# Kernel tuning notes

Measured on AMD Instinct MI355X. Metric: run time of the kernel, lower is better.

The kernel has to match this reference:

```python
import jax, jax.numpy as jnp
import numpy as np

INNER_DIM = 512
SCALE = 1.0 / np.sqrt(INNER_DIM).astype(np.float32)  # module scales by 1/sqrt(inner_dim), not head_dim


def setup_inputs() -> dict:
    key = jax.random.key(0)
    ks = jax.random.split(key, 7)
    b, n, d = 4, 4096, 512
    s = 0.02
    return {
        "x": jax.random.normal(ks[0], (b, n, d), jnp.float32),
        "y": jax.random.normal(ks[1], (b, n, d), jnp.float32),
        "Wq": jax.random.normal(ks[2], (INNER_DIM, d), jnp.float32) * s,  # torch Linear weight [out, in]
        "Wk": jax.random.normal(ks[3], (INNER_DIM, d), jnp.float32) * s,
        "Wv": jax.random.normal(ks[4], (INNER_DIM, d), jnp.float32) * s,
        "Wo": jax.random.normal(ks[5], (d, INNER_DIM), jnp.float32) * s,
        "bo": jax.random.normal(ks[6], (d,), jnp.float32) * s,
    }


def reference(x, y, Wq, Wk, Wv, Wo, bo):
    # q, k from x; v from y (bias-free projections)
    q = jnp.einsum('bnd,id->bni', x, Wq)
    k = jnp.einsum('bnd,id->bni', x, Wk)
    v = jnp.einsum('bnd,id->bni', y, Wv)
    # full [b, n, n] scores, scaled by 1/sqrt(inner_dim)
    alpha = jnp.einsum('bik,bjk->bij', q, k) * SCALE
    alpha = jax.nn.softmax(alpha, axis=-1)
    ctx = jnp.einsum('bij,bjd->bid', alpha, v)
    out = jnp.einsum('bid,od->bio', ctx, Wo) + bo
    return out
```

## Files before the change

### kernel.cpp

```cpp
#include <hip/hip_runtime.h>
#include <hip/hip_bf16.h>


typedef unsigned short u16;
typedef __bf16 bf16x8 __attribute__((ext_vector_type(8)));
typedef float f32x4 __attribute__((ext_vector_type(4)));

#define SCALE_QK 0.044194173824159216f

__device__ __forceinline__ u16 f2bf(float f) {
    __hip_bfloat16 h = __float2bfloat16(f);
    return __builtin_bit_cast(u16, h);
}

__device__ __forceinline__ void load_lds16(const void* g, void* l) {
    __builtin_amdgcn_global_load_lds(
        (const __attribute__((address_space(1))) void*)g,
        (__attribute__((address_space(3))) void*)l, 16, 0, 0);
}

__global__ void cvt2_bf16_kernel(const float* __restrict__ s0, const float* __restrict__ s1,
                                 u16* __restrict__ dst, int n8, float scale0, float scale1) {
    int i = blockIdx.x * blockDim.x + threadIdx.x;
    const float4* s4;
    float scale;
    int j;
    if (i < n8) { s4 = (const float4*)s0; scale = scale0; j = i; }
    else        { s4 = (const float4*)s1; scale = scale1; j = i - n8; }
    float4 v0 = s4[2 * j], v1 = s4[2 * j + 1];
    union { u16 u[8]; uint4 v; } o;
    o.u[0] = f2bf(v0.x * scale); o.u[1] = f2bf(v0.y * scale);
    o.u[2] = f2bf(v0.z * scale); o.u[3] = f2bf(v0.w * scale);
    o.u[4] = f2bf(v1.x * scale); o.u[5] = f2bf(v1.y * scale);
    o.u[6] = f2bf(v1.z * scale); o.u[7] = f2bf(v1.w * scale);
    ((uint4*)dst)[i] = o.v;
}

__global__ void wvo_kernel(const float* __restrict__ Wo, const float* __restrict__ Wv,
                           u16* __restrict__ Wvob) {
    int ob = blockIdx.x * 4, t = threadIdx.x;
    float a[4][2] = {{0.f, 0.f}, {0.f, 0.f}, {0.f, 0.f}, {0.f, 0.f}};
    for (int i = 0; i < 512; ++i) {
        float v0 = Wv[i * 512 + t], v1 = Wv[i * 512 + t + 256];
#pragma unroll
        for (int r = 0; r < 4; ++r) {
            float w = Wo[(ob + r) * 512 + i];
            a[r][0] += w * v0;
            a[r][1] += w * v1;
        }
    }
#pragma unroll
    for (int r = 0; r < 4; ++r) {
        Wvob[(ob + r) * 512 + t] = f2bf(a[r][0]);
        Wvob[(ob + r) * 512 + t + 256] = f2bf(a[r][1]);
    }
}

template <int DOEXP>
__launch_bounds__(512, 2)
__global__ void gemm256_kernel(const u16* __restrict__ A, const u16* __restrict__ B,
                               u16* __restrict__ Cout, int N, int lda, int ldb,
                               long long sAz, long long sBz, long long sCz) {
    __shared__ u16 lds[8][8192];

    const int tid = threadIdx.x;
    const int wave = tid >> 6, lane = tid & 63;
    const int lr = lane & 15, lg = lane >> 4;
    const int wm = wave >> 2, wn = wave & 3;
    const int rsw = (lg ^ ((lr >> 1) & 3)) << 3;

    const int gx = gridDim.x, gy = gridDim.y;
    int bid = (blockIdx.z * gy + blockIdx.y) * gx + blockIdx.x;
    const int nwg = gx * gy * gridDim.z;
    int lgc = (bid & 7) * (nwg >> 3) + (bid >> 3);
    const int bx = lgc % gx;
    int rem = lgc / gx;
    const int by = rem % gy, z = rem / gy;
    const int row0 = by * 256, col0 = bx * 256;

    const u16* Ab = A + (size_t)z * sAz;
    const u16* Bb = B + (size_t)z * sBz;

    const int rb = lane >> 2;
    const int kg8 = ((lane & 3) ^ ((rb >> 1) & 3)) << 3;

    f32x4 acc[8][4];
#pragma unroll
    for (int i = 0; i < 8; ++i)
#pragma unroll
        for (int j = 0; j < 4; ++j) acc[i][j] = (f32x4){0.f, 0.f, 0.f, 0.f};

#define STAGE_HALF(s_, slot_)                                                     \
    {                                                                             \
        const int h_ = (s_)&3, ts_ = (s_) >> 2;                                   \
        const u16* G_ = (h_ & 1) ? Bb : Ab;                                       \
        const int pan_ = (h_ & 1) ? col0 : row0;                                  \
        const int ld_ = (h_ & 1) ? ldb : lda;                                     \
        const int kofs_ = ts_ * 64 + (h_ >> 1) * 32 + kg8;                        \
        _Pragma("unroll") for (int j_ = 0; j_ < 2; ++j_) {                        \
            int r_ = (j_ * 8 + wave) * 16 + rb;                                   \
            load_lds16(G_ + (size_t)(pan_ + r_) * ld_ + kofs_,                    \
                       &lds[slot_][(j_ * 8 + wave) * 512]);                       \
        }                                                                         \
    }

    #pragma unroll
    for (int s = 0; s < 6; ++s) STAGE_HALF(s, s);
    asm volatile("s_waitcnt vmcnt(4)");
    __builtin_amdgcn_s_barrier();

#pragma unroll
    for (int i = 0; i < 4; ++i) {
#pragma unroll
        for (int m = 0; m < 4; ++m) {
            const int sub = m & 1;
            const int tp = (m >> 1) & 1;
            const int aslot = tp * 4 + 2 * sub;
            const int bslot = aslot + 1;

            bf16x8 af[8];
#pragma unroll
            for (int f = 0; f < 8; ++f) {
                int row = wm * 128 + f * 16 + lr;
                af[f] = *(const bf16x8*)&lds[aslot][row * 32 + rsw];
            }
            bf16x8 bfr[4];
#pragma unroll
            for (int f = 0; f < 4; ++f) {
                int row = wn * 64 + f * 16 + lr;
                bfr[f] = *(const bf16x8*)&lds[bslot][row * 32 + rsw];
            }

            {
                const int s0 = 8 * i + 2 * m + 6;
                if (s0 < 32) STAGE_HALF(s0, (2 * m + 6) & 7);
                if (s0 + 1 < 32) STAGE_HALF(s0 + 1, (2 * m + 7) & 7);
            }

            __builtin_amdgcn_s_barrier();

            __builtin_amdgcn_s_setprio(1);
#pragma unroll
            for (int f = 0; f < 8; ++f)
#pragma unroll
                for (int n = 0; n < 4; ++n)
                    acc[f][n] = __builtin_amdgcn_mfma_f32_16x16x32_bf16(
                        af[f], bfr[n], acc[f][n], 0, 0, 0);
            __builtin_amdgcn_s_setprio(0);

            if (sub == 1) {
                if (i == 3 && m == 1) asm volatile("s_waitcnt vmcnt(0)");
                else                  asm volatile("s_waitcnt vmcnt(4)");
            }
            __builtin_amdgcn_s_barrier();
        }
    }
#undef STAGE_HALF

    u16* C = Cout + (size_t)z * sCz;
#pragma unroll
    for (int fm = 0; fm < 8; ++fm)
#pragma unroll
        for (int fn = 0; fn < 4; ++fn)
#pragma unroll
            for (int reg = 0; reg < 4; ++reg) {
                int r = row0 + wm * 128 + fm * 16 + lg * 4 + reg;
                int c = col0 + wn * 64 + fn * 16 + lr;
                float v = acc[fm][fn][reg];
                if (DOEXP) v = __expf(v);
                C[(size_t)r * N + c] = f2bf(v);
            }
}

__launch_bounds__(512, 2)
__global__ void pv8_kernel(const u16* __restrict__ P, const u16* __restrict__ vwT,
                           float* __restrict__ part, float* __restrict__ lpart) {
    __shared__ u16 lds[8][8192];

    const int tid = threadIdx.x;
    const int wave = tid >> 6, lane = tid & 63;
    const int lr = lane & 15, lg = lane >> 4;
    const int wm = wave >> 2, wn = wave & 3;
    const int rsw = (lg ^ ((lr >> 1) & 3)) << 3;

    int bid = blockIdx.x;
    int lgc = (bid & 7) * 32 + (bid >> 3);
    const int rp = lgc & 15;
    const int t5 = lgc >> 4;
    const int cx = t5 & 1, ks = (t5 >> 1) & 1, z = t5 >> 2;
    const int row0 = rp * 256;
    const int col0 = cx * 256;

    const u16* Ab = P + (size_t)z * 16777216 + (size_t)ks * 2048;
    const u16* Bb = vwT + (size_t)z * 2097152 + (size_t)ks * 2048;

    const int rb = lane >> 2;
    const int kg8 = ((lane & 3) ^ ((rb >> 1) & 3)) << 3;

    f32x4 acc[8][4];
#pragma unroll
    for (int i = 0; i < 8; ++i)
#pragma unroll
        for (int j = 0; j < 4; ++j) acc[i][j] = (f32x4){0.f, 0.f, 0.f, 0.f};
    float rsm[8] = {0.f, 0.f, 0.f, 0.f, 0.f, 0.f, 0.f, 0.f};

#define STAGE_HALF(s_, slot_)                                                     \
    {                                                                             \
        const int h_ = (s_)&3, ts_ = (s_) >> 2;                                   \
        const u16* G_ = (h_ & 1) ? Bb : Ab;                                       \
        const int pan_ = (h_ & 1) ? col0 : row0;                                  \
        const int kofs_ = ts_ * 64 + (h_ >> 1) * 32 + kg8;                        \
        _Pragma("unroll") for (int j_ = 0; j_ < 2; ++j_) {                        \
            int r_ = (j_ * 8 + wave) * 16 + rb;                                   \
            load_lds16(G_ + (size_t)(pan_ + r_) * 4096 + kofs_,                   \
                       &lds[slot_][(j_ * 8 + wave) * 512]);                       \
        }                                                                         \
    }

    #pragma unroll
    for (int s = 0; s < 6; ++s) STAGE_HALF(s, s);
    asm volatile("s_waitcnt vmcnt(4)");
    __builtin_amdgcn_s_barrier();

    for (int i = 0; i < 16; ++i) {
#pragma unroll
        for (int m = 0; m < 4; ++m) {
            const int sub = m & 1;
            const int tp = (m >> 1) & 1;
            const int aslot = tp * 4 + 2 * sub;
            const int bslot = aslot + 1;

            bf16x8 af[8];
#pragma unroll
            for (int f = 0; f < 8; ++f) {
                int row = wm * 128 + f * 16 + lr;
                af[f] = *(const bf16x8*)&lds[aslot][row * 32 + rsw];
            }
            bf16x8 bfr[4];
#pragma unroll
            for (int f = 0; f < 4; ++f) {
                int row = wn * 64 + f * 16 + lr;
                bfr[f] = *(const bf16x8*)&lds[bslot][row * 32 + rsw];
            }

            {
                const int s0 = 8 * i + 2 * m + 6;
                if (s0 < 128) STAGE_HALF(s0, (2 * m + 6) & 7);
                if (s0 + 1 < 128) STAGE_HALF(s0 + 1, (2 * m + 7) & 7);
            }

            __builtin_amdgcn_s_barrier();

            __builtin_amdgcn_s_setprio(1);
#pragma unroll
            for (int f = 0; f < 8; ++f)
#pragma unroll
                for (int n = 0; n < 4; ++n)
                    acc[f][n] = __builtin_amdgcn_mfma_f32_16x16x32_bf16(
                        af[f], bfr[n], acc[f][n], 0, 0, 0);
            __builtin_amdgcn_s_setprio(0);

            if (wn == 0) {
#pragma unroll
                for (int f = 0; f < 8; ++f) {
                    union { bf16x8 v; unsigned u[4]; } cv;
                    cv.v = af[f];
#pragma unroll
                    for (int w = 0; w < 4; ++w)
                        rsm[f] += __uint_as_float(cv.u[w] << 16) +
                                  __uint_as_float(cv.u[w] & 0xffff0000u);
                }
            }

            if (sub == 1) {
                if (i == 15 && m == 1) asm volatile("s_waitcnt vmcnt(0)");
                else                   asm volatile("s_waitcnt vmcnt(4)");
            }
            __builtin_amdgcn_s_barrier();
        }
    }
#undef STAGE_HALF

    if (wn == 0) {
#pragma unroll
        for (int j = 0; j < 8; ++j) {
            rsm[j] += __shfl_xor(rsm[j], 16, 64);
            rsm[j] += __shfl_xor(rsm[j], 32, 64);
        }
        if (cx == 0 && lg == 0) {
            float* lp = lpart + (size_t)ks * 16384 + z * 4096 + row0 + wm * 128;
#pragma unroll
            for (int j = 0; j < 8; ++j) lp[j * 16 + lr] = rsm[j];
        }
    }

    float* O = part + (size_t)ks * 8388608 + ((size_t)z * 4096 + row0) * 512;
#pragma unroll
    for (int fm = 0; fm < 8; ++fm)
#pragma unroll
        for (int fn = 0; fn < 4; ++fn) {
            int c = col0 + wn * 64 + fn * 16 + lr;
#pragma unroll
            for (int reg = 0; reg < 4; ++reg) {
                int r = wm * 128 + fm * 16 + lg * 4 + reg;
                O[(size_t)r * 512 + c] = acc[fm][fn][reg];
            }
        }
}

template <int EPI>
__launch_bounds__(256)
__global__ void gemm_bt_kernel(const u16* __restrict__ A, const u16* __restrict__ B,
                               void* __restrict__ Cout, int N, int K, int lda, int ldb,
                               long long sAz, long long sBz, long long sCz) {
    __shared__ u16 As[2][128 * 32];
    __shared__ u16 Bs[2][128 * 32];

    const int tid = threadIdx.x;
    const int wave = tid >> 6, lane = tid & 63;
    const int lr = lane & 15, lg = lane >> 4;
    const int wr = wave >> 1, wc = wave & 1;

    const int gx = gridDim.x, gy = gridDim.y;
    int bid = (blockIdx.z * gy + blockIdx.y) * gx + blockIdx.x;
    const int nwg = gx * gy * gridDim.z;
    int lgc = (bid & 7) * (nwg >> 3) + (bid >> 3);
    const int bx = lgc % gx;
    int rem = lgc / gx;
    const int by = rem % gy, z = rem / gy;
    const int row0 = by * 128, col0 = bx * 128;

    const u16* Ab = A + (size_t)z * sAz;
    const u16* Bb = B + (size_t)z * sBz;

    f32x4 acc[4][4];
#pragma unroll
    for (int i = 0; i < 4; ++i)
#pragma unroll
        for (int j = 0; j < 4; ++j) acc[i][j] = (f32x4){0.f, 0.f, 0.f, 0.f};

    const int KT = K >> 5;

#define STAGE(bufi, kt2)                                                          \
    {                                                                             \
        _Pragma("unroll") for (int i = 0; i < 2; ++i) {                           \
            int chunk = i * 256 + tid;                                            \
            int r = chunk >> 2, c4 = chunk & 3;                                   \
            load_lds16(Ab + (size_t)(row0 + r) * lda + (kt2) * 32 + c4 * 8,       \
                       &As[bufi][(i * 256 + wave * 64) * 8]);                     \
            load_lds16(Bb + (size_t)(col0 + r) * ldb + (kt2) * 32 + c4 * 8,       \
                       &Bs[bufi][(i * 256 + wave * 64) * 8]);                     \
        }                                                                         \
    }

    STAGE(0, 0);
    int buf = 0;
    for (int kt = 0; kt < KT; ++kt) {
        __syncthreads();
        if (kt + 1 < KT) STAGE(buf ^ 1, kt + 1);

        bf16x8 af[4], bfr[4];
#pragma unroll
        for (int mf = 0; mf < 4; ++mf)
            af[mf] = *(const bf16x8*)&As[buf][(wr * 64 + mf * 16 + lr) * 32 + lg * 8];
#pragma unroll
        for (int nf = 0; nf < 4; ++nf)
            bfr[nf] = *(const bf16x8*)&Bs[buf][(wc * 64 + nf * 16 + lr) * 32 + lg * 8];
#pragma unroll
        for (int mf = 0; mf < 4; ++mf)
#pragma unroll
            for (int nf = 0; nf < 4; ++nf)
                acc[mf][nf] = __builtin_amdgcn_mfma_f32_16x16x32_bf16(
                    af[mf], bfr[nf], acc[mf][nf], 0, 0, 0);
        buf ^= 1;
    }
#undef STAGE

    const int rbase = row0 + wr * 64;
    const int cbase = col0 + wc * 64;

    if (EPI == 0) {
        u16* C = (u16*)Cout + (size_t)z * sCz;
#pragma unroll
        for (int mf = 0; mf < 4; ++mf)
#pragma unroll
            for (int nf = 0; nf < 4; ++nf)
#pragma unroll
                for (int reg = 0; reg < 4; ++reg) {
                    int r = rbase + mf * 16 + lg * 4 + reg;
                    int c = cbase + nf * 16 + lr;
                    C[(size_t)r * N + c] = f2bf(acc[mf][nf][reg]);
                }
    } else {
        u16* C = (u16*)Cout;
#pragma unroll
        for (int mf = 0; mf < 4; ++mf)
#pragma unroll
            for (int nf = 0; nf < 4; ++nf) {
                int rg = rbase + mf * 16 + lg * 4;
                int bsel = rg >> 12, rl = rg & 4095;
                int c = cbase + nf * 16 + lr;
                union { u16 u[4]; uint2 v; } o;
#pragma unroll
                for (int reg = 0; reg < 4; ++reg) o.u[reg] = f2bf(acc[mf][nf][reg]);
                *(uint2*)(C + ((size_t)bsel << 21) + ((size_t)c << 12) + rl) = o.v;
            }
    }
}

__global__ void reduce_kernel(const float* __restrict__ part,
                              const float* __restrict__ lpart,
                              const float* __restrict__ bo,
                              float* __restrict__ out) {
    int i = blockIdx.x * blockDim.x + threadIdx.x;
    int r = i >> 7, c4 = i & 127;
    float inv = 1.0f / (lpart[r] + lpart[16384 + r]);
    float4 a = ((const float4*)part)[i];
    float4 b = ((const float4*)part)[i + 2097152];
    float4 bi = ((const float4*)bo)[c4];
    float4 o;
    o.x = (a.x + b.x) * inv + bi.x;
    o.y = (a.y + b.y) * inv + bi.y;
    o.z = (a.z + b.z) * inv + bi.z;
    o.w = (a.w + b.w) * inv + bi.w;
    ((float4*)out)[i] = o;
}

extern "C" void kernel_launch(void* const* d_in, const int* in_sizes, int n_in,
                              void* d_out, int out_size, void* d_ws, size_t ws_size,
                              hipStream_t stream) {
    const float* x  = (const float*)d_in[0];
    const float* y  = (const float*)d_in[1];
    const float* Wq = (const float*)d_in[2];
    const float* Wk = (const float*)d_in[3];
    const float* Wv = (const float*)d_in[4];
    const float* Wo = (const float*)d_in[5];
    const float* bo = (const float*)d_in[6];
    float* out = (float*)d_out;

    char* ws = (char*)d_ws;
    u16*   xb   = (u16*)(ws + 0);
    u16*   qk   = (u16*)(ws + 33554432);
    float* part = (float*)(ws + 0);
    u16*   vwT  = (u16*)(ws + 67108864);
    u16*   Wqkb = (u16*)(ws + 83886080);
    u16*   Wvob = (u16*)(ws + 84934656);
    float* lpart= (float*)(ws + 86507520);
    u16*   P    = (u16*)(ws + 86638592);

    cvt2_bf16_kernel<<<8192, 256, 0, stream>>>(x, y, xb, 1048576, 1.0f, 1.0f);
    cvt2_bf16_kernel<<<256, 256, 0, stream>>>(Wq, Wk, Wqkb, 32768, SCALE_QK, 1.0f);
    wvo_kernel<<<128, 256, 0, stream>>>(Wo, Wv, Wvob);

    gemm256_kernel<0><<<dim3(4, 64, 1), 512, 0, stream>>>(xb, Wqkb, qk,
                                                          1024, 512, 512, 0, 0, 0);
    gemm_bt_kernel<1><<<dim3(4, 128, 1), 256, 0, stream>>>(xb + 8388608, Wvob, vwT,
                                                           512, 512, 512, 512, 0, 0, 0);

    gemm256_kernel<1><<<dim3(16, 16, 4), 512, 0, stream>>>(qk, qk + 512, P,
                                                           4096, 1024, 1024,
                                                           4194304, 4194304, 16777216);

    pv8_kernel<<<256, 512, 0, stream>>>(P, vwT, part, lpart);

    reduce_kernel<<<8192, 256, 0, stream>>>(part, lpart, bo, out);
}
```

Before: 317.9 us.

## Fuse prep kernels and loop batches in QK gemm with cross-batch prefetch

Merges the two conversion kernels and the Wv·Wo precompute into one prep launch, removing two launches. The QK^T exp gemm now covers all 4 batches in one persistent 256-block grid. Each block loops over the batches and prefetches the next batch's first K stages during the current batch's tail, which hides pipeline fill and drain. This cuts grid parallelism from 1024 to 256 blocks, so there is one wave of blocks per CU with less latency hiding from oversubscription.

Result: slower. 376.4 us (+18.4%).

```diff
diff --git a/kernel.cpp b/kernel.cpp
--- a/kernel.cpp
+++ b/kernel.cpp
@@ -19,44 +19,52 @@
         (__attribute__((address_space(3))) void*)l, 16, 0, 0);
 }
 
-__global__ void cvt2_bf16_kernel(const float* __restrict__ s0, const float* __restrict__ s1,
-                                 u16* __restrict__ dst, int n8, float scale0, float scale1) {
-    int i = blockIdx.x * blockDim.x + threadIdx.x;
-    const float4* s4;
-    float scale;
-    int j;
-    if (i < n8) { s4 = (const float4*)s0; scale = scale0; j = i; }
-    else        { s4 = (const float4*)s1; scale = scale1; j = i - n8; }
-    float4 v0 = s4[2 * j], v1 = s4[2 * j + 1];
-    union { u16 u[8]; uint4 v; } o;
-    o.u[0] = f2bf(v0.x * scale); o.u[1] = f2bf(v0.y * scale);
-    o.u[2] = f2bf(v0.z * scale); o.u[3] = f2bf(v0.w * scale);
-    o.u[4] = f2bf(v1.x * scale); o.u[5] = f2bf(v1.y * scale);
-    o.u[6] = f2bf(v1.z * scale); o.u[7] = f2bf(v1.w * scale);
-    ((uint4*)dst)[i] = o.v;
-}
-
-__global__ void wvo_kernel(const float* __restrict__ Wo, const float* __restrict__ Wv,
-                           u16* __restrict__ Wvob) {
-    int ob = blockIdx.x * 4, t = threadIdx.x;
-    float a[4][2] = {{0.f, 0.f}, {0.f, 0.f}, {0.f, 0.f}, {0.f, 0.f}};
-    for (int i = 0; i < 512; ++i) {
-        float v0 = Wv[i * 512 + t], v1 = Wv[i * 512 + t + 256];
+__global__ void prep_kernel(const float* __restrict__ x, const float* __restrict__ y,
+                            const float* __restrict__ Wq, const float* __restrict__ Wk,
+                            const float* __restrict__ Wo, const float* __restrict__ Wv,
+                            u16* __restrict__ xb, u16* __restrict__ Wqkb,
+                            u16* __restrict__ Wvob) {
+    const int b = blockIdx.x, tid = threadIdx.x;
+    if (b < 8448) {
+        const float *s0, *s1;
+        u16* dst;
+        int n8, i;
+        float sc0, sc1;
+        if (b < 8192) { s0 = x;  s1 = y;  dst = xb;   n8 = 1048576; sc0 = 1.f;      sc1 = 1.f; i = b * 256 + tid; }
+        else          { s0 = Wq; s1 = Wk; dst = Wqkb; n8 = 32768;   sc0 = SCALE_QK; sc1 = 1.f; i = (b - 8192) * 256 + tid; }
+        const float4* s4;
+        float scale;
+        int j;
+        if (i < n8) { s4 = (const float4*)s0; scale = sc0; j = i; }
+        else        { s4 = (const float4*)s1; scale = sc1; j = i - n8; }
+        float4 v0 = s4[2 * j], v1 = s4[2 * j + 1];
+        union { u16 u[8]; uint4 v; } o;
+        o.u[0] = f2bf(v0.x * scale); o.u[1] = f2bf(v0.y * scale);
+        o.u[2] = f2bf(v0.z * scale); o.u[3] = f2bf(v0.w * scale);
+        o.u[4] = f2bf(v1.x * scale); o.u[5] = f2bf(v1.y * scale);
+        o.u[6] = f2bf(v1.z * scale); o.u[7] = f2bf(v1.w * scale);
+        ((uint4*)dst)[i] = o.v;
+    } else {
+        int ob = (b - 8448) * 4, t = tid;
+        float a[4][2] = {{0.f, 0.f}, {0.f, 0.f}, {0.f, 0.f}, {0.f, 0.f}};
+        for (int i = 0; i < 512; ++i) {
+            float v0 = Wv[i * 512 + t], v1 = Wv[i * 512 + t + 256];
+#pragma unroll
+            for (int r = 0; r < 4; ++r) {
+                float w = Wo[(ob + r) * 512 + i];
+                a[r][0] += w * v0;
+                a[r][1] += w * v1;
+            }
+        }
 #pragma unroll
         for (int r = 0; r < 4; ++r) {
-            float w = Wo[(ob + r) * 512 + i];
-            a[r][0] += w * v0;
-            a[r][1] += w * v1;
-        }
-    }
-#pragma unroll
-    for (int r = 0; r < 4; ++r) {
-        Wvob[(ob + r) * 512 + t] = f2bf(a[r][0]);
-        Wvob[(ob + r) * 512 + t + 256] = f2bf(a[r][1]);
-    }
-}
-
-template <int DOEXP>
+            Wvob[(ob + r) * 512 + t] = f2bf(a[r][0]);
+            Wvob[(ob + r) * 512 + t + 256] = f2bf(a[r][1]);
+        }
+    }
+}
+
+template <int DOEXP, int TPB>
 __launch_bounds__(512, 2)
 __global__ void gemm256_kernel(const u16* __restrict__ A, const u16* __restrict__ B,
                                u16* __restrict__ Cout, int N, int lda, int ldb,
@@ -70,30 +78,19 @@
     const int rsw = (lg ^ ((lr >> 1) & 3)) << 3;
 
     const int gx = gridDim.x, gy = gridDim.y;
-    int bid = (blockIdx.z * gy + blockIdx.y) * gx + blockIdx.x;
-    const int nwg = gx * gy * gridDim.z;
+    int bid = blockIdx.y * gx + blockIdx.x;
+    const int nwg = gx * gy;
     int lgc = (bid & 7) * (nwg >> 3) + (bid >> 3);
-    const int bx = lgc % gx;
-    int rem = lgc / gx;
-    const int by = rem % gy, z = rem / gy;
+    const int bx = lgc % gx, by = lgc / gx;
     const int row0 = by * 256, col0 = bx * 256;
-
-    const u16* Ab = A + (size_t)z * sAz;
-    const u16* Bb = B + (size_t)z * sBz;
 
     const int rb = lane >> 2;
     const int kg8 = ((lane & 3) ^ ((rb >> 1) & 3)) << 3;
 
-    f32x4 acc[8][4];
-#pragma unroll
-    for (int i = 0; i < 8; ++i)
-#pragma unroll
-        for (int j = 0; j < 4; ++j) acc[i][j] = (f32x4){0.f, 0.f, 0.f, 0.f};
-
-#define STAGE_HALF(s_, slot_)                                                     \
+#define STAGE_HALF(Ab_, Bb_, s_, slot_)                                           \
     {                                                                             \
         const int h_ = (s_)&3, ts_ = (s_) >> 2;                                   \
-        const u16* G_ = (h_ & 1) ? Bb : Ab;                                       \
+        const u16* G_ = (h_ & 1) ? (Bb_) : (Ab_);                                 \
         const int pan_ = (h_ & 1) ? col0 : row0;                                  \
         const int ld_ = (h_ & 1) ? ldb : lda;                                     \
         const int kofs_ = ts_ * 64 + (h_ >> 1) * 32 + kg8;                        \
@@ -105,71 +102,91 @@
     }
 
     #pragma unroll
-    for (int s = 0; s < 6; ++s) STAGE_HALF(s, s);
+    for (int s = 0; s < 6; ++s) STAGE_HALF(A, B, s, s);
     asm volatile("s_waitcnt vmcnt(4)");
     __builtin_amdgcn_s_barrier();
 
-#pragma unroll
-    for (int i = 0; i < 4; ++i) {
-#pragma unroll
-        for (int m = 0; m < 4; ++m) {
-            const int sub = m & 1;
-            const int tp = (m >> 1) & 1;
-            const int aslot = tp * 4 + 2 * sub;
-            const int bslot = aslot + 1;
-
-            bf16x8 af[8];
-#pragma unroll
-            for (int f = 0; f < 8; ++f) {
-                int row = wm * 128 + f * 16 + lr;
-                af[f] = *(const bf16x8*)&lds[aslot][row * 32 + rsw];
-            }
-            bf16x8 bfr[4];
-#pragma unroll
-            for (int f = 0; f < 4; ++f) {
-                int row = wn * 64 + f * 16 + lr;
-                bfr[f] = *(const bf16x8*)&lds[bslot][row * 32 + rsw];
-            }
-
-            {
-                const int s0 = 8 * i + 2 * m + 6;
-                if (s0 < 32) STAGE_HALF(s0, (2 * m + 6) & 7);
-                if (s0 + 1 < 32) STAGE_HALF(s0 + 1, (2 * m + 7) & 7);
-            }
-
-            __builtin_amdgcn_s_barrier();
-
-            __builtin_amdgcn_s_setprio(1);
-#pragma unroll
-            for (int f = 0; f < 8; ++f)
-#pragma unroll
-                for (int n = 0; n < 4; ++n)
-                    acc[f][n] = __builtin_amdgcn_mfma_f32_16x16x32_bf16(
-                        af[f], bfr[n], acc[f][n], 0, 0, 0);
-            __builtin_amdgcn_s_setprio(0);
-
-            if (sub == 1) {
-                if (i == 3 && m == 1) asm volatile("s_waitcnt vmcnt(0)");
-                else                  asm volatile("s_waitcnt vmcnt(4)");
-            }
-            __builtin_amdgcn_s_barrier();
-        }
+    for (int t = 0; t < TPB; ++t) {
+        const u16* Ab = A + (size_t)t * sAz;
+        const u16* Bb = B + (size_t)t * sBz;
+        const u16* Abn = A + (size_t)(t + 1) * sAz;
+        const u16* Bbn = B + (size_t)(t + 1) * sBz;
+
+        f32x4 acc[8][4];
+#pragma unroll
+        for (int i = 0; i < 8; ++i)
+#pragma unroll
+            for (int j = 0; j < 4; ++j) acc[i][j] = (f32x4){0.f, 0.f, 0.f, 0.f};
+
+#pragma unroll
+        for (int i = 0; i < 4; ++i) {
+#pragma unroll
+            for (int m = 0; m < 4; ++m) {
+                const int sub = m & 1;
+                const int tp = (m >> 1) & 1;
+                const int aslot = tp * 4 + 2 * sub;
+                const int bslot = aslot + 1;
+
+                bf16x8 af[8];
+#pragma unroll
+                for (int f = 0; f < 8; ++f) {
+                    int row = wm * 128 + f * 16 + lr;
+                    af[f] = *(const bf16x8*)&lds[aslot][row * 32 + rsw];
+                }
+                bf16x8 bfr[4];
+#pragma unroll
+                for (int f = 0; f < 4; ++f) {
+                    int row = wn * 64 + f * 16 + lr;
+                    bfr[f] = *(const bf16x8*)&lds[bslot][row * 32 + rsw];
+                }
+
+                {
+                    const int s0 = 8 * i + 2 * m + 6;
+                    if (s0 < 32) {
+                        STAGE_HALF(Ab, Bb, s0, (2 * m + 6) & 7);
+                        STAGE_HALF(Ab, Bb, s0 + 1, (2 * m + 7) & 7);
+                    } else if (t + 1 < TPB) {
+                        STAGE_HALF(Abn, Bbn, s0 - 32, (2 * m + 6) & 7);
+                        STAGE_HALF(Abn, Bbn, s0 - 31, (2 * m + 7) & 7);
+                    }
+                }
+
+                __builtin_amdgcn_s_barrier();
+
+                __builtin_amdgcn_s_setprio(1);
+#pragma unroll
+                for (int f = 0; f < 8; ++f)
+#pragma unroll
+                    for (int n = 0; n < 4; ++n)
+                        acc[f][n] = __builtin_amdgcn_mfma_f32_16x16x32_bf16(
+                            af[f], bfr[n], acc[f][n], 0, 0, 0);
+                __builtin_amdgcn_s_setprio(0);
+
+                if (sub == 1) {
+                    if (t == TPB - 1 && i == 3 && m == 1)
+                        asm volatile("s_waitcnt vmcnt(0)");
+                    else
+                        asm volatile("s_waitcnt vmcnt(4)");
+                }
+                __builtin_amdgcn_s_barrier();
+            }
+        }
+
+        u16* C = Cout + (size_t)t * sCz;
+#pragma unroll
+        for (int fm = 0; fm < 8; ++fm)
+#pragma unroll
+            for (int fn = 0; fn < 4; ++fn)
+#pragma unroll
+                for (int reg = 0; reg < 4; ++reg) {
+                    int r = row0 + wm * 128 + fm * 16 + lg * 4 + reg;
+                    int c = col0 + wn * 64 + fn * 16 + lr;
+                    float v = acc[fm][fn][reg];
+                    if (DOEXP) v = __expf(v);
+                    C[(size_t)r * N + c] = f2bf(v);
+                }
     }
 #undef STAGE_HALF
-
-    u16* C = Cout + (size_t)z * sCz;
-#pragma unroll
-    for (int fm = 0; fm < 8; ++fm)
-#pragma unroll
-        for (int fn = 0; fn < 4; ++fn)
-#pragma unroll
-            for (int reg = 0; reg < 4; ++reg) {
-                int r = row0 + wm * 128 + fm * 16 + lg * 4 + reg;
-                int c = col0 + wn * 64 + fn * 16 + lr;
-                float v = acc[fm][fn][reg];
-                if (DOEXP) v = __expf(v);
-                C[(size_t)r * N + c] = f2bf(v);
-            }
 }
 
 __launch_bounds__(512, 2)
@@ -448,16 +465,14 @@
     float* lpart= (float*)(ws + 86507520);
     u16*   P    = (u16*)(ws + 86638592);
 
-    cvt2_bf16_kernel<<<8192, 256, 0, stream>>>(x, y, xb, 1048576, 1.0f, 1.0f);
-    cvt2_bf16_kernel<<<256, 256, 0, stream>>>(Wq, Wk, Wqkb, 32768, SCALE_QK, 1.0f);
-    wvo_kernel<<<128, 256, 0, stream>>>(Wo, Wv, Wvob);
-
-    gemm256_kernel<0><<<dim3(4, 64, 1), 512, 0, stream>>>(xb, Wqkb, qk,
+    prep_kernel<<<8576, 256, 0, stream>>>(x, y, Wq, Wk, Wo, Wv, xb, Wqkb, Wvob);
+
+    gemm256_kernel<0, 1><<<dim3(4, 64), 512, 0, stream>>>(xb, Wqkb, qk,
                                                           1024, 512, 512, 0, 0, 0);
     gemm_bt_kernel<1><<<dim3(4, 128, 1), 256, 0, stream>>>(xb + 8388608, Wvob, vwT,
                                                            512, 512, 512, 512, 0, 0, 0);
 
-    gemm256_kernel<1><<<dim3(16, 16, 4), 512, 0, stream>>>(qk, qk + 512, P,
+    gemm256_kernel<1, 4><<<dim3(16, 16), 512, 0, stream>>>(qk, qk + 512, P,
                                                            4096, 1024, 1024,
                                                            4194304, 4194304, 16777216);
 
```
